# Kernel tuning notes

Hardware: AMD Instinct MI355X
Metric: run time of the kernel (lower is better)

The kernel has to match this reference:

```python
import jax, jax.numpy as jnp
import numpy as np

B, N, F = 8, 1024, 256
OUT, REL = 256, 16
NADJ = 7  # ((2 relations + consecutive) * 2 for backward) + self link


def setup_inputs() -> dict:
    key = jax.random.key(0)
    k0, k1, k2, k3, k4 = jax.random.split(key, 5)
    features = jax.random.normal(k0, (B, N, F), dtype=jnp.float32)
    A1 = jax.random.uniform(k1, (B, N, N), dtype=jnp.float32)
    A2 = jax.random.uniform(k2, (B, N, N), dtype=jnp.float32)
    # learned params: one (F+REL, OUT) weight per adjacency matrix, edge embeddings init 'ones', bias (N, OUT)
    W = jax.random.normal(k3, (NADJ, F + REL, OUT), dtype=jnp.float32) * 0.05
    W_edges = jnp.ones((NADJ, REL), dtype=jnp.float32)
    b = jax.random.uniform(k4, (N, OUT), dtype=jnp.float32, minval=-0.05, maxval=0.05)
    return {"features": features, "A1": A1, "A2": A2, "W": W, "W_edges": W_edges, "b": b}


def reference(features, A1, A2, W, W_edges, b):
    # eye = A[0] * zeros(N) + eye(N)  -> batch-broadcast identity [B,N,N]
    eye = jnp.zeros_like(A1) + jnp.eye(N, dtype=A1.dtype)
    # original rolls along axis 0 (batch) of the broadcast identity (faithful replication)
    shifted = jnp.roll(eye, 1, axis=0)
    A_fwd = [A1, A2, shifted]                      # relations + consecutive link
    A_list = A_fwd + [jnp.swapaxes(a, 1, 2) for a in A_fwd]  # backward links
    A_list.append(eye)                             # self links
    A = jnp.stack(A_list, axis=0)                  # [R,B,N,N]

    # concat(features, tile(W_edges[r])) @ W[r] == features @ W[r][:F] + W_edges[r] @ W[r][F:]
    HW = jnp.einsum('bnf,rfo->rbno', features, W[:, :F]) \
         + jnp.einsum('rd,rdo->ro', W_edges, W[:, F:])[:, None, None, :]  # [R,B,N,OUT]
    AHW = jnp.einsum('rbnm,rbmo->rbno', A, HW)     # batched adjacency matmul
    out = jnp.max(AHW, axis=0) + b                 # max-aggregate over relations, add bias
    return out                                     # activation = linear
```

## Files before the change

kernel.cpp:

```cpp
#include <hip/hip_runtime.h>
#include <hip/hip_bf16.h>

#define B_ 8
#define N_ 1024
#define F_ 256
#define OUT_ 256
#define REL_ 16
#define NADJ_ 7

typedef __attribute__((ext_vector_type(8))) _Float16 f16x8;
typedef __attribute__((ext_vector_type(4))) float f32x4;

__device__ __forceinline__ void gll16(const _Float16* g, _Float16* l) {
    __builtin_amdgcn_global_load_lds(
        (const __attribute__((address_space(1))) void*)g,
        (__attribute__((address_space(3))) void*)l, 16, 0, 0);
}

__constant__ const int c_perm[7] = {0, 1, 3, 4, 2, 5, 6};

__global__ __launch_bounds__(256) void prep_kernel(const float* __restrict__ W,
                                                   const float* __restrict__ We,
                                                   const float* __restrict__ feat,
                                                   float* __restrict__ cb,
                                                   _Float16* __restrict__ WTp,
                                                   _Float16* __restrict__ Fe) {
    int bid = blockIdx.x, tid = threadIdx.x;
    if (bid < 7) {
        int idx = bid * 256 + tid;
        int j = idx / OUT_, o = idx % OUT_;
        int r = c_perm[j];
        const float* Wr = W + (size_t)r * (F_ + REL_) * OUT_;
        float s = 0.f;
#pragma unroll
        for (int d = 0; d < REL_; ++d) s += We[r * REL_ + d] * Wr[(F_ + d) * OUT_ + o];
        cb[idx] = s;
    } else if (bid < 1799) {
        int idx = (bid - 7) * 256 + tid;
        int j = idx >> 16, rem = idx & 65535, o = rem >> 8, f = rem & 255;
        int r = c_perm[j];
        WTp[idx] = (_Float16)W[((size_t)r * (F_ + REL_) + f) * OUT_ + o];
    } else {
        int i = (bid - 1799) * 256 + tid;
        size_t base = (size_t)i * 8;
        float4 a = *(const float4*)(feat + base);
        float4 b = *(const float4*)(feat + base + 4);
        f16x8 v = {(_Float16)a.x, (_Float16)a.y, (_Float16)a.z, (_Float16)a.w,
                   (_Float16)b.x, (_Float16)b.y, (_Float16)b.z, (_Float16)b.w};
        *(f16x8*)(Fe + base) = v;
    }
}

__global__ __launch_bounds__(256) void convAB_kernel(const float* __restrict__ A1,
                                                     const float* __restrict__ A2,
                                                     _Float16* __restrict__ Af) {
    __shared__ _Float16 T[4096];
    int z = blockIdx.z, s = z >> 3, b = z & 7;
    const float* src = (s ? A2 : A1) + (size_t)b * N_ * N_;
    int k0 = blockIdx.x * 64, n0 = blockIdx.y * 64;
    int t = threadIdx.x;
    int r = t >> 2, cs = (t & 3) * 16;
    const float* sp = src + (size_t)(k0 + r) * N_ + n0 + cs;
    _Float16 v[16];
#pragma unroll
    for (int j = 0; j < 16; j += 4) {
        float4 f = *(const float4*)(sp + j);
        v[j] = (_Float16)f.x; v[j + 1] = (_Float16)f.y;
        v[j + 2] = (_Float16)f.z; v[j + 3] = (_Float16)f.w;
    }
    const size_t slab = (size_t)8 * N_ * N_;
    {
        _Float16* dst = Af + (size_t)s * slab + (size_t)b * N_ * N_ + (size_t)(k0 + r) * N_ + n0 + cs;
        f16x8 p0 = {v[0], v[1], v[2], v[3], v[4], v[5], v[6], v[7]};
        f16x8 p1 = {v[8], v[9], v[10], v[11], v[12], v[13], v[14], v[15]};
        *(f16x8*)dst = p0;
        *(f16x8*)(dst + 8) = p1;
    }
#pragma unroll
    for (int j = 0; j < 16; ++j) {
        int n = cs + j;
        int sw = ((n ^ (n >> 3)) & 7) << 3;
        T[n * 64 + (r ^ sw)] = v[j];
    }
    __syncthreads();
    {
        int n = t >> 2, i2 = (t & 3) * 16;
        int sw = ((n ^ (n >> 3)) & 7) << 3;
        f16x8 q0 = *(const f16x8*)&T[n * 64 + (i2 ^ sw)];
        f16x8 q1 = *(const f16x8*)&T[n * 64 + ((i2 + 8) ^ sw)];
        _Float16* dt = Af + (size_t)(2 + s) * slab + (size_t)b * N_ * N_ + (size_t)(n0 + n) * N_ + k0 + i2;
        *(f16x8*)dt = q0;
        *(f16x8*)(dt + 8) = q1;
    }
}

template <int MODE>
__global__ __launch_bounds__(256) void gemm128(
    const _Float16* __restrict__ A, const _Float16* __restrict__ Bt,
    _Float16* __restrict__ C, const float* __restrict__ bias,
    int K, int lda, int ldb, int ldc, int zdiv,
    size_t sAhi, size_t sAlo, size_t sBhi, size_t sBlo, size_t sChi, size_t sClo) {
    __shared__ _Float16 As[128 * 32];
    __shared__ _Float16 Bs[128 * 32];
    const int z = blockIdx.z, zh = z / zdiv, zl = z % zdiv;
    A += sAhi * zh + sAlo * zl;
    Bt += sBhi * zh + sBlo * zl;
    C += sChi * zh + sClo * zl;
    const int tid = threadIdx.x;
    const int m0 = blockIdx.y * 128, n0 = blockIdx.x * 128;
    const int wave = tid >> 6, lane = tid & 63, lm = lane & 15, q = lane >> 4;
    const int wr = (wave >> 1) * 64, wc = (wave & 1) * 64;
    const int srow = tid >> 2, sk = (tid & 3) * 8;
    const _Float16* ga0 = A + (size_t)(m0 + srow) * lda + sk;
    const _Float16* ga1 = ga0 + (size_t)64 * lda;
    const _Float16* gb0 = Bt + (size_t)(n0 + srow) * ldb + sk;
    const _Float16* gb1 = gb0 + (size_t)64 * ldb;
    _Float16* la0 = As + tid * 8;
    _Float16* la1 = As + 2048 + tid * 8;
    _Float16* lb0 = Bs + tid * 8;
    _Float16* lb1 = Bs + 2048 + tid * 8;

    f32x4 acc[4][4] = {};
    for (int k0 = 0; k0 < K; k0 += 32) {
        gll16(ga0 + k0, la0);
        gll16(ga1 + k0, la1);
        gll16(gb0 + k0, lb0);
        gll16(gb1 + k0, lb1);
        __syncthreads();
        f16x8 af[4], bf[4];
#pragma unroll
        for (int i = 0; i < 4; ++i) af[i] = *(const f16x8*)(As + (wr + i * 16 + lm) * 32 + q * 8);
#pragma unroll
        for (int j = 0; j < 4; ++j) bf[j] = *(const f16x8*)(Bs + (wc + j * 16 + lm) * 32 + q * 8);
#pragma unroll
        for (int i = 0; i < 4; ++i)
#pragma unroll
            for (int j = 0; j < 4; ++j)
                acc[i][j] = __builtin_amdgcn_mfma_f32_16x16x32_f16(af[i], bf[j], acc[i][j], 0, 0, 0);
        __syncthreads();
    }
    if (MODE) bias += (size_t)z * 256;
#pragma unroll
    for (int i = 0; i < 4; ++i)
#pragma unroll
        for (int j = 0; j < 4; ++j)
#pragma unroll
            for (int g = 0; g < 4; ++g) {
                int row = wr + i * 16 + q * 4 + g;
                int col = wc + j * 16 + lm;
                float v = acc[i][j][g];
                if (MODE == 1) v += bias[n0 + col];
                if (MODE == 2) v += bias[m0 + row];
                C[(size_t)(m0 + row) * ldc + (n0 + col)] = (_Float16)v;
            }
}

__global__ __launch_bounds__(256) void max_kernel(const _Float16* __restrict__ AHW,
                                                  const _Float16* __restrict__ HWN,
                                                  const float* __restrict__ bias,
                                                  float* __restrict__ out) {
    size_t i = ((size_t)blockIdx.x * 256 + threadIdx.x) * 8;
    const size_t slab = (size_t)B_ * N_ * OUT_;
    float m[8];
    f16x8 v = *(const f16x8*)(AHW + i);
#pragma unroll
    for (int e = 0; e < 8; ++e) m[e] = (float)v[e];
#pragma unroll
    for (int rr = 1; rr < 4; ++rr) {
        f16x8 w = *(const f16x8*)(AHW + rr * slab + i);
#pragma unroll
        for (int e = 0; e < 8; ++e) m[e] = fmaxf(m[e], (float)w[e]);
    }
#pragma unroll
    for (int j = 0; j < 3; ++j) {
        f16x8 w = *(const f16x8*)(HWN + j * slab + i);
#pragma unroll
        for (int e = 0; e < 8; ++e) m[e] = fmaxf(m[e], (float)w[e]);
    }
    size_t bidx = i & ((size_t)N_ * OUT_ - 1);
    float4 b0 = *(const float4*)(bias + bidx);
    float4 b1 = *(const float4*)(bias + bidx + 4);
    float4 o0 = {m[0] + b0.x, m[1] + b0.y, m[2] + b0.z, m[3] + b0.w};
    float4 o1 = {m[4] + b1.x, m[5] + b1.y, m[6] + b1.z, m[7] + b1.w};
    *(float4*)(out + i) = o0;
    *(float4*)(out + i + 4) = o1;
}

__global__ void cbias_kernel(const float* __restrict__ W, const float* __restrict__ We,
                             float* __restrict__ c) {
    int idx = blockIdx.x * 256 + threadIdx.x;
    if (idx >= NADJ_ * OUT_) return;
    int r = idx / OUT_, o = idx % OUT_;
    const float* Wr = W + (size_t)r * (F_ + REL_) * OUT_;
    float s = 0.f;
#pragma unroll
    for (int d = 0; d < REL_; ++d) s += We[r * REL_ + d] * Wr[(F_ + d) * OUT_ + o];
    c[idx] = s;
}

__global__ __launch_bounds__(256) void hw_kernel(const float* __restrict__ feat,
                                                 const float* __restrict__ W,
                                                 const float* __restrict__ cb,
                                                 _Float16* __restrict__ HWb) {
    __shared__ _Float16 As[64][32];
    __shared__ _Float16 Bs[64][32];
    const int mt = blockIdx.x, ct = blockIdx.y;
    const int tid = threadIdx.x, wave = tid >> 6, lane = tid & 63;
    const int r = (ct * 64) / OUT_;
    const int o0 = (ct * 64) % OUT_;
    const float* Bg = W + (size_t)r * (F_ + REL_) * OUT_ + o0;
    const int m0 = mt * 64;
    const int lm = lane & 15, q = lane >> 4;
    f32x4 acc[4] = {};
    for (int k0 = 0; k0 < F_; k0 += 32) {
        {
            int seg = (tid & 3) * 8, m = tid >> 2;
            const float* src = feat + (size_t)(m0 + m) * F_ + k0 + seg;
#pragma unroll
            for (int j = 0; j < 8; ++j) As[m][seg + j] = (_Float16)src[j];
        }
        {
            int kk = tid >> 3, ns = (tid & 7) * 8;
            const float* src = Bg + (size_t)(k0 + kk) * OUT_ + ns;
#pragma unroll
            for (int j = 0; j < 8; ++j) Bs[ns + j][kk] = (_Float16)src[j];
        }
        __syncthreads();
        f16x8 a = *(const f16x8*)&As[wave * 16 + lm][q * 8];
#pragma unroll
        for (int c4 = 0; c4 < 4; ++c4) {
            f16x8 b = *(const f16x8*)&Bs[c4 * 16 + lm][q * 8];
            acc[c4] = __builtin_amdgcn_mfma_f32_16x16x32_f16(a, b, acc[c4], 0, 0, 0);
        }
        __syncthreads();
    }
#pragma unroll
    for (int c4 = 0; c4 < 4; ++c4)
#pragma unroll
        for (int g = 0; g < 4; ++g) {
            int row = wave * 16 + (lane >> 4) * 4 + g;
            int col = c4 * 16 + lm;
            float v = acc[c4][g] + cb[r * OUT_ + o0 + col];
            HWb[((size_t)r * B_ * N_ + m0 + row) * OUT_ + o0 + col] = (_Float16)v;
        }
}

__global__ __launch_bounds__(256) void agg_kernel(const float* __restrict__ A1,
                                                  const float* __restrict__ A2,
                                                  const _Float16* __restrict__ HWb,
                                                  const float* __restrict__ bias,
                                                  float* __restrict__ out) {
    __shared__ _Float16 As[64][32];
    __shared__ _Float16 Bs[64][32];
    const int b = blockIdx.z, nt = blockIdx.y, ot = blockIdx.x;
    const int tid = threadIdx.x, wave = tid >> 6, lane = tid & 63;
    const int n0 = nt * 64, o0 = ot * 64;
    const int lm = lane & 15, q = lane >> 4;
    const size_t rstride = (size_t)B_ * N_ * OUT_;
    f32x4 mx[4];
#pragma unroll
    for (int i = 0; i < 4; ++i) mx[i] = f32x4{-1e30f, -1e30f, -1e30f, -1e30f};
#pragma unroll 1
    for (int rr = 0; rr < 4; ++rr) {
        const float* Ag = ((rr & 1) ? A2 : A1) + (size_t)b * N_ * N_;
        const bool tr = (rr >= 2);
        const int r = (rr < 2) ? rr : rr + 1;
        const _Float16* Bg = HWb + (size_t)r * rstride + (size_t)b * N_ * OUT_ + o0;
        f32x4 acc[4] = {};
        for (int k0 = 0; k0 < N_; k0 += 32) {
            if (!tr) {
                int seg = (tid & 3) * 8, m = tid >> 2;
                const float* src = Ag + (size_t)(n0 + m) * N_ + k0 + seg;
#pragma unroll
                for (int j = 0; j < 8; ++j) As[m][seg + j] = (_Float16)src[j];
            } else {
                int kk = tid >> 3, ms = (tid & 7) * 8;
                const float* src = Ag + (size_t)(k0 + kk) * N_ + n0 + ms;
#pragma unroll
                for (int j = 0; j < 8; ++j) As[ms + j][kk] = (_Float16)src[j];
            }
            {
                int kk = tid >> 3, ns = (tid & 7) * 8;
                const _Float16* src = Bg + (size_t)(k0 + kk) * OUT_ + ns;
#pragma unroll
                for (int j = 0; j < 8; ++j) Bs[ns + j][kk] = src[j];
            }
            __syncthreads();
            f16x8 a = *(const f16x8*)&As[wave * 16 + lm][q * 8];
#pragma unroll
            for (int c4 = 0; c4 < 4; ++c4) {
                f16x8 bb = *(const f16x8*)&Bs[c4 * 16 + lm][q * 8];
                acc[c4] = __builtin_amdgcn_mfma_f32_16x16x32_f16(a, bb, acc[c4], 0, 0, 0);
            }
            __syncthreads();
        }
#pragma unroll
        for (int c4 = 0; c4 < 4; ++c4)
#pragma unroll
            for (int g = 0; g < 4; ++g) mx[c4][g] = fmaxf(mx[c4][g], acc[c4][g]);
    }
#pragma unroll
    for (int c4 = 0; c4 < 4; ++c4)
#pragma unroll
        for (int g = 0; g < 4; ++g) {
            int row = wave * 16 + (lane >> 4) * 4 + g;
            int col = c4 * 16 + lm;
            size_t pos = ((size_t)b * N_ + n0 + row) * OUT_ + o0 + col;
            float v = mx[c4][g];
            v = fmaxf(v, (float)HWb[2 * rstride + pos]);
            v = fmaxf(v, (float)HWb[5 * rstride + pos]);
            v = fmaxf(v, (float)HWb[6 * rstride + pos]);
            out[pos] = v + bias[((size_t)(n0 + row)) * OUT_ + o0 + col];
        }
}

extern "C" void kernel_launch(void* const* d_in, const int* in_sizes, int n_in,
                              void* d_out, int out_size, void* d_ws, size_t ws_size,
                              hipStream_t stream) {
    const float* feat = (const float*)d_in[0];
    const float* A1   = (const float*)d_in[1];
    const float* A2   = (const float*)d_in[2];
    const float* W    = (const float*)d_in[3];
    const float* We   = (const float*)d_in[4];
    const float* bias = (const float*)d_in[5];
    float* out = (float*)d_out;

    const size_t OFF_CB   = 0;
    const size_t OFF_WT   = 8192;
    const size_t OFF_FE   = 1048576;
    const size_t OFF_AF   = 5242880;
    const size_t OFF_HWT  = 72351744;
    const size_t OFF_HWN  = 89128960;
    const size_t OFF_AHW  = 101711872;
    const size_t WS_NEEDED = 118489088;

    if (ws_size >= WS_NEEDED) {
        float*    cbp = (float*)((char*)d_ws + OFF_CB);
        _Float16* WTp = (_Float16*)((char*)d_ws + OFF_WT);
        _Float16* Fe  = (_Float16*)((char*)d_ws + OFF_FE);
        _Float16* Af  = (_Float16*)((char*)d_ws + OFF_AF);
        _Float16* HWT = (_Float16*)((char*)d_ws + OFF_HWT);
        _Float16* HWN = (_Float16*)((char*)d_ws + OFF_HWN);
        _Float16* AHW = (_Float16*)((char*)d_ws + OFF_AHW);

        prep_kernel<<<2823, 256, 0, stream>>>(W, We, feat, cbp, WTp, Fe);
        convAB_kernel<<<dim3(16, 16, 16), 256, 0, stream>>>(A1, A2, Af);

        gemm128<1><<<dim3(2, 64, 3), 256, 0, stream>>>(
            Fe, WTp + (size_t)4 * 65536, HWN, cbp + 4 * 256,
            F_, F_, F_, OUT_, 1,
            0, 0, 65536, 0, (size_t)8192 * 256, 0);
        gemm128<2><<<dim3(64, 2, 4), 256, 0, stream>>>(
            WTp, Fe, HWT, cbp,
            F_, F_, F_, 8192, 1,
            65536, 0, 0, 0, (size_t)256 * 8192, 0);
        gemm128<0><<<dim3(2, 8, 32), 256, 0, stream>>>(
            Af, HWT, AHW, nullptr,
            N_, N_, 8192, OUT_, 8,
            (size_t)8 * 1048576, 1048576,
            (size_t)256 * 8192, 1024,
            (size_t)8 * 262144, 262144);
        max_kernel<<<1024, 256, 0, stream>>>(AHW, HWN, bias, out);
    } else {
        float* cb = (float*)d_ws;
        _Float16* HWb = (_Float16*)((char*)d_ws + 8192);
        cbias_kernel<<<7, 256, 0, stream>>>(W, We, cb);
        hw_kernel<<<dim3(128, 28), 256, 0, stream>>>(feat, W, cb, HWb);
        agg_kernel<<<dim3(4, 16, 8), 256, 0, stream>>>(A1, A2, HWb, bias, out);
    }
}
```

Measured before the change: 195.1 us.

## Merge prep kernels and HW GEMMs, reorder aggregation GEMM blocks for L2 reuse

Combines the adjacency conversion and weight/feature prep into one launch, and merges the two small HW GEMMs (transposed and normal outputs) into a single launch with seven z-slices. The aggregation GEMM moves to a 1D grid whose block index pairs the two column tiles of the same A row-block next to each other, so the shared A tile is likely still in L2 when the second block reads it. The aim is to cut launch overhead and tail effects and improve cache reuse. In exchange, the merged kernels carry divergent block roles and the prep branch has a larger LDS footprint.

```diff
diff --git a/kernel.cpp b/kernel.cpp
--- a/kernel.cpp
+++ b/kernel.cpp
@@ -19,15 +19,56 @@
 
 __constant__ const int c_perm[7] = {0, 1, 3, 4, 2, 5, 6};
 
-__global__ __launch_bounds__(256) void prep_kernel(const float* __restrict__ W,
-                                                   const float* __restrict__ We,
-                                                   const float* __restrict__ feat,
-                                                   float* __restrict__ cb,
-                                                   _Float16* __restrict__ WTp,
-                                                   _Float16* __restrict__ Fe) {
-    int bid = blockIdx.x, tid = threadIdx.x;
-    if (bid < 7) {
-        int idx = bid * 256 + tid;
+__global__ __launch_bounds__(256) void convprep_kernel(const float* __restrict__ A1,
+                                                       const float* __restrict__ A2,
+                                                       const float* __restrict__ W,
+                                                       const float* __restrict__ We,
+                                                       const float* __restrict__ feat,
+                                                       _Float16* __restrict__ Af,
+                                                       float* __restrict__ cb,
+                                                       _Float16* __restrict__ WTp,
+                                                       _Float16* __restrict__ Fe) {
+    __shared__ _Float16 T[4096];
+    int bid = blockIdx.x, t = threadIdx.x;
+    if (bid < 4096) {
+        int z = bid >> 8, s = z >> 3, b = z & 7;
+        const float* src = (s ? A2 : A1) + (size_t)b * N_ * N_;
+        int k0 = (bid & 15) * 64, n0 = ((bid >> 4) & 15) * 64;
+        int r = t >> 2, cs = (t & 3) * 16;
+        const float* sp = src + (size_t)(k0 + r) * N_ + n0 + cs;
+        _Float16 v[16];
+#pragma unroll
+        for (int j = 0; j < 16; j += 4) {
+            float4 f = *(const float4*)(sp + j);
+            v[j] = (_Float16)f.x; v[j + 1] = (_Float16)f.y;
+            v[j + 2] = (_Float16)f.z; v[j + 3] = (_Float16)f.w;
+        }
+        const size_t slab = (size_t)8 * N_ * N_;
+        {
+            _Float16* dst = Af + (size_t)s * slab + (size_t)b * N_ * N_ + (size_t)(k0 + r) * N_ + n0 + cs;
+            f16x8 p0 = {v[0], v[1], v[2], v[3], v[4], v[5], v[6], v[7]};
+            f16x8 p1 = {v[8], v[9], v[10], v[11], v[12], v[13], v[14], v[15]};
+            *(f16x8*)dst = p0;
+            *(f16x8*)(dst + 8) = p1;
+        }
+#pragma unroll
+        for (int j = 0; j < 16; ++j) {
+            int n = cs + j;
+            int sw = ((n ^ (n >> 3)) & 7) << 3;
+            T[n * 64 + (r ^ sw)] = v[j];
+        }
+        __syncthreads();
+        {
+            int n = t >> 2, i2 = (t & 3) * 16;
+            int sw = ((n ^ (n >> 3)) & 7) << 3;
+            f16x8 q0 = *(const f16x8*)&T[n * 64 + (i2 ^ sw)];
+            f16x8 q1 = *(const f16x8*)&T[n * 64 + ((i2 + 8) ^ sw)];
+            _Float16* dt = Af + (size_t)(2 + s) * slab + (size_t)b * N_ * N_ + (size_t)(n0 + n) * N_ + k0 + i2;
+            *(f16x8*)dt = q0;
+            *(f16x8*)(dt + 8) = q1;
+        }
+    } else if (bid < 4103) {
+        int idx = (bid - 4096) * 256 + t;
         int j = idx / OUT_, o = idx % OUT_;
         int r = c_perm[j];
         const float* Wr = W + (size_t)r * (F_ + REL_) * OUT_;
@@ -35,13 +76,13 @@
 #pragma unroll
         for (int d = 0; d < REL_; ++d) s += We[r * REL_ + d] * Wr[(F_ + d) * OUT_ + o];
         cb[idx] = s;
-    } else if (bid < 1799) {
-        int idx = (bid - 7) * 256 + tid;
+    } else if (bid < 5895) {
+        int idx = (bid - 4103) * 256 + t;
         int j = idx >> 16, rem = idx & 65535, o = rem >> 8, f = rem & 255;
         int r = c_perm[j];
         WTp[idx] = (_Float16)W[((size_t)r * (F_ + REL_) + f) * OUT_ + o];
     } else {
-        int i = (bid - 1799) * 256 + tid;
+        int i = (bid - 5895) * 256 + t;
         size_t base = (size_t)i * 8;
         float4 a = *(const float4*)(feat + base);
         float4 b = *(const float4*)(feat + base + 4);
@@ -51,77 +92,34 @@
     }
 }
 
-__global__ __launch_bounds__(256) void convAB_kernel(const float* __restrict__ A1,
-                                                     const float* __restrict__ A2,
-                                                     _Float16* __restrict__ Af) {
-    __shared__ _Float16 T[4096];
-    int z = blockIdx.z, s = z >> 3, b = z & 7;
-    const float* src = (s ? A2 : A1) + (size_t)b * N_ * N_;
-    int k0 = blockIdx.x * 64, n0 = blockIdx.y * 64;
-    int t = threadIdx.x;
-    int r = t >> 2, cs = (t & 3) * 16;
-    const float* sp = src + (size_t)(k0 + r) * N_ + n0 + cs;
-    _Float16 v[16];
-#pragma unroll
-    for (int j = 0; j < 16; j += 4) {
-        float4 f = *(const float4*)(sp + j);
-        v[j] = (_Float16)f.x; v[j + 1] = (_Float16)f.y;
-        v[j + 2] = (_Float16)f.z; v[j + 3] = (_Float16)f.w;
-    }
-    const size_t slab = (size_t)8 * N_ * N_;
-    {
-        _Float16* dst = Af + (size_t)s * slab + (size_t)b * N_ * N_ + (size_t)(k0 + r) * N_ + n0 + cs;
-        f16x8 p0 = {v[0], v[1], v[2], v[3], v[4], v[5], v[6], v[7]};
-        f16x8 p1 = {v[8], v[9], v[10], v[11], v[12], v[13], v[14], v[15]};
-        *(f16x8*)dst = p0;
-        *(f16x8*)(dst + 8) = p1;
-    }
-#pragma unroll
-    for (int j = 0; j < 16; ++j) {
-        int n = cs + j;
-        int sw = ((n ^ (n >> 3)) & 7) << 3;
-        T[n * 64 + (r ^ sw)] = v[j];
-    }
-    __syncthreads();
-    {
-        int n = t >> 2, i2 = (t & 3) * 16;
-        int sw = ((n ^ (n >> 3)) & 7) << 3;
-        f16x8 q0 = *(const f16x8*)&T[n * 64 + (i2 ^ sw)];
-        f16x8 q1 = *(const f16x8*)&T[n * 64 + ((i2 + 8) ^ sw)];
-        _Float16* dt = Af + (size_t)(2 + s) * slab + (size_t)b * N_ * N_ + (size_t)(n0 + n) * N_ + k0 + i2;
-        *(f16x8*)dt = q0;
-        *(f16x8*)(dt + 8) = q1;
-    }
-}
-
-template <int MODE>
-__global__ __launch_bounds__(256) void gemm128(
-    const _Float16* __restrict__ A, const _Float16* __restrict__ Bt,
-    _Float16* __restrict__ C, const float* __restrict__ bias,
-    int K, int lda, int ldb, int ldc, int zdiv,
-    size_t sAhi, size_t sAlo, size_t sBhi, size_t sBlo, size_t sChi, size_t sClo) {
+__global__ __launch_bounds__(256) void hw7_kernel(const _Float16* __restrict__ Fe,
+                                                  const _Float16* __restrict__ WTp,
+                                                  const float* __restrict__ cb,
+                                                  _Float16* __restrict__ HWT,
+                                                  _Float16* __restrict__ HWN) {
     __shared__ _Float16 As[128 * 32];
     __shared__ _Float16 Bs[128 * 32];
-    const int z = blockIdx.z, zh = z / zdiv, zl = z % zdiv;
-    A += sAhi * zh + sAlo * zl;
-    Bt += sBhi * zh + sBlo * zl;
-    C += sChi * zh + sClo * zl;
+    const int z = blockIdx.z, bx = blockIdx.x, by = blockIdx.y;
+    const bool tr = (z < 4);
+    const _Float16* A  = tr ? (WTp + (size_t)z * 65536) : Fe;
+    const _Float16* Bt = tr ? Fe : (WTp + (size_t)z * 65536);
+    const int m0 = (tr ? by : bx) * 128;
+    const int n0 = (tr ? bx : by) * 128;
     const int tid = threadIdx.x;
-    const int m0 = blockIdx.y * 128, n0 = blockIdx.x * 128;
     const int wave = tid >> 6, lane = tid & 63, lm = lane & 15, q = lane >> 4;
     const int wr = (wave >> 1) * 64, wc = (wave & 1) * 64;
     const int srow = tid >> 2, sk = (tid & 3) * 8;
-    const _Float16* ga0 = A + (size_t)(m0 + srow) * lda + sk;
-    const _Float16* ga1 = ga0 + (size_t)64 * lda;
-    const _Float16* gb0 = Bt + (size_t)(n0 + srow) * ldb + sk;
-    const _Float16* gb1 = gb0 + (size_t)64 * ldb;
+    const _Float16* ga0 = A + (size_t)(m0 + srow) * F_ + sk;
+    const _Float16* ga1 = ga0 + (size_t)64 * F_;
+    const _Float16* gb0 = Bt + (size_t)(n0 + srow) * F_ + sk;
+    const _Float16* gb1 = gb0 + (size_t)64 * F_;
     _Float16* la0 = As + tid * 8;
     _Float16* la1 = As + 2048 + tid * 8;
     _Float16* lb0 = Bs + tid * 8;
     _Float16* lb1 = Bs + 2048 + tid * 8;
 
     f32x4 acc[4][4] = {};
-    for (int k0 = 0; k0 < K; k0 += 32) {
+    for (int k0 = 0; k0 < F_; k0 += 32) {
         gll16(ga0 + k0, la0);
         gll16(ga1 + k0, la1);
         gll16(gb0 + k0, lb0);
@@ -139,7 +137,82 @@
                 acc[i][j] = __builtin_amdgcn_mfma_f32_16x16x32_f16(af[i], bf[j], acc[i][j], 0, 0, 0);
         __syncthreads();
     }
-    if (MODE) bias += (size_t)z * 256;
+    const float* cbz = cb + (size_t)z * 256;
+    if (tr) {
+        _Float16* C = HWT + (size_t)z * ((size_t)256 * 8192);
+#pragma unroll
+        for (int i = 0; i < 4; ++i)
+#pragma unroll
+            for (int j = 0; j < 4; ++j)
+#pragma unroll
+                for (int g = 0; g < 4; ++g) {
+                    int row = wr + i * 16 + q * 4 + g;
+                    int col = wc + j * 16 + lm;
+                    float v = acc[i][j][g] + cbz[m0 + row];
+                    C[(size_t)(m0 + row) * 8192 + (n0 + col)] = (_Float16)v;
+                }
+    } else {
+        _Float16* C = HWN + (size_t)(z - 4) * ((size_t)8192 * 256);
+#pragma unroll
+        for (int i = 0; i < 4; ++i)
+#pragma unroll
+            for (int j = 0; j < 4; ++j)
+#pragma unroll
+                for (int g = 0; g < 4; ++g) {
+                    int row = wr + i * 16 + q * 4 + g;
+                    int col = wc + j * 16 + lm;
+                    float v = acc[i][j][g] + cbz[n0 + col];
+                    C[(size_t)(m0 + row) * 256 + (n0 + col)] = (_Float16)v;
+                }
+    }
+}
+
+__global__ __launch_bounds__(256) void p2_kernel(const _Float16* __restrict__ Af,
+                                                 const _Float16* __restrict__ HWT,
+                                                 _Float16* __restrict__ AHW) {
+    __shared__ _Float16 As[128 * 32];
+    __shared__ _Float16 Bs[128 * 32];
+    const int d = blockIdx.x;
+    const int member = (d >> 3) & 1;
+    const int p = (d & 7) | ((d >> 4) << 3);
+    const int mt = p & 7, zz = p >> 3;
+    const int rr = zz >> 3, b = zz & 7;
+    const _Float16* A  = Af + (size_t)rr * (8 * 1048576) + (size_t)b * 1048576;
+    const _Float16* Bt = HWT + (size_t)rr * (256 * 8192) + (size_t)b * 1024;
+    _Float16* C = AHW + (size_t)rr * (8 * 262144) + (size_t)b * 262144;
+    const int m0 = mt * 128, n0 = member * 128;
+    const int tid = threadIdx.x;
+    const int wave = tid >> 6, lane = tid & 63, lm = lane & 15, q = lane >> 4;
+    const int wr = (wave >> 1) * 64, wc = (wave & 1) * 64;
+    const int srow = tid >> 2, sk = (tid & 3) * 8;
+    const _Float16* ga0 = A + (size_t)(m0 + srow) * N_ + sk;
+    const _Float16* ga1 = ga0 + (size_t)64 * N_;
+    const _Float16* gb0 = Bt + (size_t)(n0 + srow) * 8192 + sk;
+    const _Float16* gb1 = gb0 + (size_t)64 * 8192;
+    _Float16* la0 = As + tid * 8;
+    _Float16* la1 = As + 2048 + tid * 8;
+    _Float16* lb0 = Bs + tid * 8;
+    _Float16* lb1 = Bs + 2048 + tid * 8;
+
+    f32x4 acc[4][4] = {};
+    for (int k0 = 0; k0 < N_; k0 += 32) {
+        gll16(ga0 + k0, la0);
+        gll16(ga1 + k0, la1);
+        gll16(gb0 + k0, lb0);
+        gll16(gb1 + k0, lb1);
+        __syncthreads();
+        f16x8 af[4], bf[4];
+#pragma unroll
+        for (int i = 0; i < 4; ++i) af[i] = *(const f16x8*)(As + (wr + i * 16 + lm) * 32 + q * 8);
+#pragma unroll
+        for (int j = 0; j < 4; ++j) bf[j] = *(const f16x8*)(Bs + (wc + j * 16 + lm) * 32 + q * 8);
+#pragma unroll
+        for (int i = 0; i < 4; ++i)
+#pragma unroll
+            for (int j = 0; j < 4; ++j)
+                acc[i][j] = __builtin_amdgcn_mfma_f32_16x16x32_f16(af[i], bf[j], acc[i][j], 0, 0, 0);
+        __syncthreads();
+    }
 #pragma unroll
     for (int i = 0; i < 4; ++i)
 #pragma unroll
@@ -148,10 +221,7 @@
             for (int g = 0; g < 4; ++g) {
                 int row = wr + i * 16 + q * 4 + g;
                 int col = wc + j * 16 + lm;
-                float v = acc[i][j][g];
-                if (MODE == 1) v += bias[n0 + col];
-                if (MODE == 2) v += bias[m0 + row];
-                C[(size_t)(m0 + row) * ldc + (n0 + col)] = (_Float16)v;
+                C[(size_t)(m0 + row) * 256 + (n0 + col)] = (_Float16)acc[i][j][g];
             }
 }
 
@@ -343,23 +413,9 @@
         _Float16* HWN = (_Float16*)((char*)d_ws + OFF_HWN);
         _Float16* AHW = (_Float16*)((char*)d_ws + OFF_AHW);
 
-        prep_kernel<<<2823, 256, 0, stream>>>(W, We, feat, cbp, WTp, Fe);
-        convAB_kernel<<<dim3(16, 16, 16), 256, 0, stream>>>(A1, A2, Af);
-
-        gemm128<1><<<dim3(2, 64, 3), 256, 0, stream>>>(
-            Fe, WTp + (size_t)4 * 65536, HWN, cbp + 4 * 256,
-            F_, F_, F_, OUT_, 1,
-            0, 0, 65536, 0, (size_t)8192 * 256, 0);
-        gemm128<2><<<dim3(64, 2, 4), 256, 0, stream>>>(
-            WTp, Fe, HWT, cbp,
-            F_, F_, F_, 8192, 1,
-            65536, 0, 0, 0, (size_t)256 * 8192, 0);
-        gemm128<0><<<dim3(2, 8, 32), 256, 0, stream>>>(
-            Af, HWT, AHW, nullptr,
-            N_, N_, 8192, OUT_, 8,
-            (size_t)8 * 1048576, 1048576,
-            (size_t)256 * 8192, 1024,
-            (size_t)8 * 262144, 262144);
+        convprep_kernel<<<6919, 256, 0, stream>>>(A1, A2, W, We, feat, Af, cbp, WTp, Fe);
+        hw7_kernel<<<dim3(64, 2, 7), 256, 0, stream>>>(Fe, WTp, cbp, HWT, HWN);
+        p2_kernel<<<512, 256, 0, stream>>>(Af, HWT, AHW);
         max_kernel<<<1024, 256, 0, stream>>>(AHW, HWN, bias, out);
     } else {
         float* cb = (float*)d_ws;
```

New measurement: 179.1 us. 8.2% less time.
